# Kernel optimization log

Hardware: AMD Instinct MI355X
Metric: run time of the kernel (lower is better)

Reference implementation:

```python
import jax, jax.numpy as jnp
import numpy as np

B, IN_CH, OUT_CH, H, W = 2, 256, 128, 96, 96
KS = 3  # deformable kernel size


def _conv2d(x, w, b=None, stride=1, padding=0):
    out = jax.lax.conv_general_dilated(
        x, w, (stride, stride), [(padding, padding), (padding, padding)],
        dimension_numbers=('NCHW', 'OIHW', 'NCHW'))
    if b is not None:
        out = out + b[None, :, None, None]
    return out


def _up2_bilinear_ac(x):
    b, c, h, w = x.shape
    H2, W2 = 2 * h, 2 * w
    ys = jnp.arange(H2, dtype=x.dtype) * ((h - 1) / (H2 - 1))
    xs = jnp.arange(W2, dtype=x.dtype) * ((w - 1) / (W2 - 1))
    y0 = jnp.floor(ys).astype(jnp.int32); y1 = jnp.minimum(y0 + 1, h - 1)
    x0 = jnp.floor(xs).astype(jnp.int32); x1 = jnp.minimum(x0 + 1, w - 1)
    wy = (ys - y0.astype(x.dtype))[None, None, :, None]
    wx = (xs - x0.astype(x.dtype))[None, None, None, :]
    rows = x[:, :, y0, :] * (1 - wy) + x[:, :, y1, :] * wy
    return rows[:, :, :, x0] * (1 - wx) + rows[:, :, :, x1] * wx


def _deform_conv(x, pw, pb, cw, ks=3):
    # DeformConv2d with padding=0, stride=1, modulation=False
    b, c, Hx, Wx = x.shape
    N = ks * ks
    off = jnp.transpose(_conv2d(x, pw, pb, stride=1, padding=1), (0, 2, 3, 1))  # [b,h,w,2N]
    h, w = off.shape[1], off.shape[2]
    r = (ks - 1) // 2
    pn_x, pn_y = jnp.meshgrid(jnp.arange(-r, r + 1), jnp.arange(-r, r + 1), indexing='ij')
    # p = p_0 (starts at 1, per torch code) + p_n + offset; x-coord first half, y-coord second half
    px = off[..., :N] + pn_x.ravel().astype(x.dtype) + jnp.arange(1, h + 1, dtype=x.dtype)[None, :, None, None]
    py = off[..., N:] + pn_y.ravel().astype(x.dtype) + jnp.arange(1, w + 1, dtype=x.dtype)[None, None, :, None]
    fx, fy = jnp.floor(px), jnp.floor(py)  # detached in torch; floor grad is 0 anyway
    x_lt = jnp.clip(fx, 0, Hx - 1); y_lt = jnp.clip(fy, 0, Wx - 1)
    x_rb = jnp.clip(fx + 1, 0, Hx - 1); y_rb = jnp.clip(fy + 1, 0, Wx - 1)
    pxc = jnp.clip(px, 0, Hx - 1); pyc = jnp.clip(py, 0, Wx - 1)
    g_lt = (1 + (x_lt - pxc)) * (1 + (y_lt - pyc))
    g_rb = (1 - (x_rb - pxc)) * (1 - (y_rb - pyc))
    g_lb = (1 + (x_lt - pxc)) * (1 - (y_rb - pyc))
    g_rt = (1 - (x_rb - pxc)) * (1 + (y_lt - pyc))
    x_flat = x.reshape(b, c, Hx * Wx)
    gather = jax.vmap(lambda xf, ix: xf[:, ix])  # [c,HW],[M] -> [c,M], vmapped over batch

    def take(qx, qy):
        idx = (qx.astype(jnp.int32) * Wx + qy.astype(jnp.int32)).reshape(b, -1)
        return gather(x_flat, idx).reshape(b, c, h, w, N)

    x_off = (g_lt[:, None] * take(x_lt, y_lt) + g_rb[:, None] * take(x_rb, y_rb)
             + g_lb[:, None] * take(x_lt, y_rb) + g_rt[:, None] * take(x_rb, y_lt))
    # _reshape_x_offset: [b,c,h,w,kx,ky] -> [b,c,h*ks,w*ks]
    x_off = x_off.reshape(b, c, h, w, ks, ks).transpose(0, 1, 2, 4, 3, 5).reshape(b, c, h * ks, w * ks)
    return _conv2d(x_off, cw, stride=ks)  # kernel=ks, stride=ks, no bias


def _bn_relu(x, g, be, eps=1e-5):
    # training-mode BatchNorm2d (biased batch variance) + ReLU
    m = x.mean(axis=(0, 2, 3), keepdims=True)
    v = x.var(axis=(0, 2, 3), keepdims=True)
    return jax.nn.relu((x - m) / jnp.sqrt(v + eps) * g[None, :, None, None] + be[None, :, None, None])


def setup_inputs() -> dict:
    key = jax.random.key(0)
    ks = jax.random.split(key, 16)
    f = jnp.float32
    return {
        'x1': jax.random.normal(ks[0], (B, OUT_CH, H, W), f),
        'x2': jax.random.normal(ks[1], (B, IN_CH, H // 2, W // 2), f),
        'chW': jax.random.normal(ks[2], (OUT_CH, IN_CH, 3, 3), f) * 0.02,
        'chB': jnp.zeros((OUT_CH,), f),
        'p1W': jax.random.normal(ks[3], (2 * KS * KS, IN_CH, 3, 3), f) * 0.01,
        'p1B': jax.random.normal(ks[4], (2 * KS * KS,), f) * 0.01,
        'c1W': jax.random.normal(ks[5], (OUT_CH, IN_CH, KS, KS), f) * 0.02,
        'bn1g': jnp.ones((OUT_CH,), f),
        'bn1b': jnp.zeros((OUT_CH,), f),
        'p2W': jax.random.normal(ks[6], (2 * KS * KS, OUT_CH, 3, 3), f) * 0.01,
        'p2B': jax.random.normal(ks[7], (2 * KS * KS,), f) * 0.01,
        'c2W': jax.random.normal(ks[8], (OUT_CH, OUT_CH, KS, KS), f) * 0.02,
        'bn2g': jnp.ones((OUT_CH,), f),
        'bn2b': jnp.zeros((OUT_CH,), f),
    }


def reference(x1, x2, chW, chB, p1W, p1B, c1W, bn1g, bn1b, p2W, p2B, c2W, bn2g, bn2b):
    x2u = _up2_bilinear_ac(x2)                                    # [B,IN_CH,H,W]
    x2c = jax.nn.relu(_conv2d(x2u, chW, chB, stride=1, padding=1))  # halve_channel -> [B,OUT_CH,H,W]
    # F.pad of x1 is a no-op here (shapes already match)
    x = jnp.concatenate([x2c, x1], axis=1)                        # [B,IN_CH,H,W]
    y = _bn_relu(_deform_conv(x, p1W, p1B, c1W, KS), bn1g, bn1b)  # [B,OUT_CH,H,W]
    y = _bn_relu(_deform_conv(y, p2W, p2B, c2W, KS), bn2g, bn2b)  # [B,OUT_CH,H,W]
    return y
```

## Files before the change

### kernel.cpp

```cpp
#include <hip/hip_runtime.h>
#include <hip/hip_bf16.h>

#define Bn 2
#define INCH 256
#define OUTCH 128
#define Hs 96
#define Ws 96
#define HW (Hs*Ws)
#define N9 9

typedef __attribute__((ext_vector_type(8))) short bf16x8;
typedef __attribute__((ext_vector_type(4))) float f32x4;

static __device__ inline ushort bfbits(float v) {
    __hip_bfloat16 h = __float2bfloat16(v);
    return *reinterpret_cast<ushort*>(&h);
}
static __device__ inline float bf2f(ushort u) {
    __hip_bfloat16 h = *reinterpret_cast<__hip_bfloat16*>(&u);
    return __bfloat162float(h);
}
static __device__ inline uint packu(ushort lo, ushort hi) {
    return (uint)lo | ((uint)hi << 16);
}
static __device__ inline float rchi(uint u) { return __uint_as_float(u << 16); }
static __device__ inline float rclo(uint u) { return __uint_as_float(u & 0xffff0000u); }

template<int C>
__global__ void up2_nhwc_kernel(const float* __restrict__ in, uint* __restrict__ out) {
    __shared__ float t[32][33];
    constexpr int PB = HW / 32;
    int blk = blockIdx.x;
    int p0 = (blk % PB) * 32;
    int c0 = ((blk / PB) % (C / 32)) * 32;
    int b = blk / (PB * (C / 32));
    int tp = threadIdx.x & 31, tg = threadIdx.x >> 5;
    int p = p0 + tp;
    int xo = p % Ws, yo = p / Ws;
    const float s = 47.0f / 95.0f;
    float yf = yo * s, xf = xo * s;
    int y0 = (int)floorf(yf); int y1 = min(y0 + 1, 47);
    int x0 = (int)floorf(xf); int x1 = min(x0 + 1, 47);
    float wy = yf - (float)y0, wx = xf - (float)x0;
    #pragma unroll
    for (int r = 0; r < 4; r++) {
        int c = c0 + tg + r * 8;
        const float* pp = in + ((size_t)b * C + c) * 2304;
        float r0 = pp[y0*48 + x0] * (1.f - wy) + pp[y1*48 + x0] * wy;
        float r1 = pp[y0*48 + x1] * (1.f - wy) + pp[y1*48 + x1] * wy;
        t[tg + r * 8][tp] = r0 * (1.f - wx) + r1 * wx;
    }
    __syncthreads();
    #pragma unroll
    for (int r = 0; r < 4; r++) {
        int po = p0 + tg + r * 8;
        float v = t[tp][tg + r * 8];
        ushort h = bfbits(v);
        ushort l = bfbits(v - bf2f(h));
        out[((size_t)b * HW + po) * C + c0 + tp] = packu(h, l);
    }
}

__global__ void combine_t_kernel(const float* __restrict__ ph0, const float* __restrict__ ph1,
                                 const float* __restrict__ x1, const float* __restrict__ bias,
                                 float* __restrict__ xcat, uint* __restrict__ xcatT) {
    __shared__ float t[32][33];
    constexpr int PB = HW / 32;
    int blk = blockIdx.x;
    int p0 = (blk % PB) * 32;
    int c0 = ((blk / PB) % (INCH / 32)) * 32;
    int b = blk / (PB * (INCH / 32));
    int tp = threadIdx.x & 31, tg = threadIdx.x >> 5;
    #pragma unroll
    for (int r = 0; r < 4; r++) {
        int c = c0 + tg + r * 8;
        float v;
        if (c < OUTCH) {
            size_t i = ((size_t)b * OUTCH + c) * HW + p0 + tp;
            v = fmaxf(ph0[i] + ph1[i] + bias[c], 0.f);
        } else {
            v = x1[((size_t)b * OUTCH + (c - OUTCH)) * HW + p0 + tp];
        }
        t[tg + r * 8][tp] = v;
        xcat[((size_t)b * INCH + c) * HW + p0 + tp] = v;
    }
    __syncthreads();
    #pragma unroll
    for (int r = 0; r < 4; r++) {
        int po = p0 + tg + r * 8;
        float v = t[tp][tg + r * 8];
        ushort h = bfbits(v);
        ushort l = bfbits(v - bf2f(h));
        xcatT[((size_t)b * HW + po) * INCH + c0 + tp] = packu(h, l);
    }
}

__global__ void bnapply_t_kernel(const float* __restrict__ p0, const float* __restrict__ p1,
                                 const float* __restrict__ mv, const float* __restrict__ g,
                                 const float* __restrict__ be,
                                 float* __restrict__ y, uint* __restrict__ yT) {
    __shared__ float t[32][33];
    constexpr int PB = HW / 32;
    int blk = blockIdx.x;
    int p0x = (blk % PB) * 32;
    int c0 = ((blk / PB) % (OUTCH / 32)) * 32;
    int b = blk / (PB * (OUTCH / 32));
    int tp = threadIdx.x & 31, tg = threadIdx.x >> 5;
    #pragma unroll
    for (int r = 0; r < 4; r++) {
        int c = c0 + tg + r * 8;
        size_t i = ((size_t)b * OUTCH + c) * HW + p0x + tp;
        float m = mv[c], vv = mv[OUTCH + c];
        float x = p0[i] + p1[i];
        float rr = fmaxf((x - m) / sqrtf(vv + 1e-5f) * g[c] + be[c], 0.f);
        t[tg + r * 8][tp] = rr;
        y[i] = rr;
    }
    __syncthreads();
    #pragma unroll
    for (int r = 0; r < 4; r++) {
        int po = p0x + tg + r * 8;
        float v = t[tp][tg + r * 8];
        ushort h = bfbits(v);
        ushort l = bfbits(v - bf2f(h));
        yT[((size_t)b * HW + po) * OUTCH + c0 + tp] = packu(h, l);
    }
}

template<int CIN, int SPLIT>
__global__ void offconv_kernel(const float* __restrict__ in, const float* __restrict__ w,
                               float* __restrict__ part) {
    constexpr int CS = CIN / SPLIT;
    constexpr int BPS = Bn * HW / 256;
    int s = blockIdx.x / BPS;
    int p = (blockIdx.x % BPS) * 256 + threadIdx.x;
    int b = p / HW; int pin = p % HW;
    int i = pin / Ws, j = pin % Ws;
    const float* ib = in + ((size_t)b * CIN + s * CS) * HW;
    const float* wb = w + (size_t)s * CS * N9;
    float acc[18];
    #pragma unroll
    for (int o = 0; o < 18; o++) acc[o] = 0.f;
    for (int c = 0; c < CS; c++) {
        float v[9];
        #pragma unroll
        for (int n = 0; n < 9; n++) {
            int rr = i + n / 3 - 1, cc = j + n % 3 - 1;
            v[n] = (rr >= 0 && rr < Hs && cc >= 0 && cc < Ws) ? ib[(size_t)c * HW + rr * Ws + cc] : 0.f;
        }
        const float* wc = wb + (size_t)c * N9;
        #pragma unroll
        for (int o = 0; o < 18; o++) {
            #pragma unroll
            for (int n = 0; n < 9; n++) acc[o] += wc[(size_t)o * CIN * N9 + n] * v[n];
        }
    }
    #pragma unroll
    for (int o = 0; o < 18; o++)
        part[(((size_t)s * Bn + b) * 18 + o) * HW + pin] = acc[o];
}

template<int SPLIT>
__global__ void offreduce_kernel(const float* __restrict__ part, const float* __restrict__ bias,
                                 float* __restrict__ off) {
    int idx = blockIdx.x * blockDim.x + threadIdx.x;
    const int total = Bn * 18 * HW;
    if (idx >= total) return;
    int pin = idx % HW;
    int o = (idx / HW) % 18;
    int b = idx / (18 * HW);
    float a = bias[o];
    #pragma unroll
    for (int s = 0; s < SPLIT; s++) a += part[(((size_t)s * Bn + b) * 18 + o) * HW + pin];
    off[((size_t)b * 18 + o) * HW + pin] = a;
}

template<int CIN>
__global__ void wprep_big_kernel(const float* __restrict__ cw, ushort* __restrict__ wp) {
    int e = blockIdx.x * 256 + threadIdx.x;
    if (e >= CIN * 9 * 128) return;
    int kl = e & 31, oc = (e >> 5) & 127, k32 = e >> 12;
    int k = k32 * 32 + kl;
    int n = k / CIN, c = k & (CIN - 1);
    float v = cw[((size_t)oc * CIN + c) * 9 + n];
    ushort h = bfbits(v);
    wp[e] = h;
    wp[e + CIN * 9 * 128] = bfbits(v - bf2f(h));
}

__global__ void mkparams_kernel(const float* __restrict__ off, int4* __restrict__ pidx,
                                float4* __restrict__ pw) {
    int e = blockIdx.x * blockDim.x + threadIdx.x;
    const int total = Bn * HW * N9;
    if (e >= total) return;
    int n = e % N9;
    int p = e / N9;
    int j = p % Ws;
    int i = (p / Ws) % Hs;
    int b = p / HW;
    float ox = off[((size_t)b * 18 + n) * HW + i * Ws + j];
    float oy = off[((size_t)b * 18 + 9 + n) * HW + i * Ws + j];
    float px = ox + (float)(n / 3 - 1) + (float)(i + 1);
    float py = oy + (float)(n % 3 - 1) + (float)(j + 1);
    float fx = floorf(px), fy = floorf(py);
    float x_lt = fminf(fmaxf(fx,       0.f), 95.f);
    float x_rb = fminf(fmaxf(fx + 1.f, 0.f), 95.f);
    float y_lt = fminf(fmaxf(fy,       0.f), 95.f);
    float y_rb = fminf(fmaxf(fy + 1.f, 0.f), 95.f);
    float pxc  = fminf(fmaxf(px, 0.f), 95.f);
    float pyc  = fminf(fmaxf(py, 0.f), 95.f);
    float g_lt = (1.f + (x_lt - pxc)) * (1.f + (y_lt - pyc));
    float g_rb = (1.f - (x_rb - pxc)) * (1.f - (y_rb - pyc));
    float g_lb = (1.f + (x_lt - pxc)) * (1.f - (y_rb - pyc));
    float g_rt = (1.f - (x_rb - pxc)) * (1.f + (y_lt - pyc));
    int ilt = (int)x_lt * Ws + (int)y_lt;
    int irb = (int)x_rb * Ws + (int)y_rb;
    int ilb = (int)x_lt * Ws + (int)y_rb;
    int irt = (int)x_rb * Ws + (int)y_lt;
    pidx[e] = make_int4(ilt, irb, ilb, irt);
    pw[e]   = make_float4(g_lt, g_rb, g_lb, g_rt);
}

template<int CIN, bool DEFORM, bool SPLIT3>
__global__ void mgemm_big_kernel(const uint* __restrict__ xT, const ushort* __restrict__ wp,
                                 const int4* __restrict__ pidx, const float4* __restrict__ pw,
                                 float* __restrict__ p0, float* __restrict__ p1) {
    constexpr int KS = CIN * 9 / 2;
    constexpr int NSTEP = KS / 64;
    constexpr int PX = 32;
    constexpr int TILES = Bn * HW / PX;
    constexpr int CPX = 2 * TILES / 8;
    __shared__ ushort Ah[2][PX][80];
    __shared__ ushort Al[2][PX][80];
    __shared__ int4  sidx[PX * N9];
    __shared__ float4 ssw[PX * N9];

    int tid = threadIdx.x;
    int bid = blockIdx.x;
    int swz = (bid & 7) * CPX + (bid >> 3);
    int s = swz / TILES;
    int t = swz % TILES;
    int p0x = t * PX;
    int b = p0x / HW;
    int pin = p0x % HW;
    int irow = pin / Ws, j0 = pin % Ws;

    if constexpr (DEFORM) {
        for (int e = tid; e < PX * N9; e += 256) {
            sidx[e] = pidx[(size_t)p0x * N9 + e];
            ssw[e]  = pw[(size_t)p0x * N9 + e];
        }
        __syncthreads();
    }
    const uint* xbT = xT + (size_t)b * HW * CIN;
    const ushort* wlo = wp + (size_t)CIN * 9 * 128;
    int w = tid >> 6, lane = tid & 63;
    int lg = lane >> 4, l15 = lane & 15;
    int fpx = tid >> 4, fc4 = tid & 15;

    f32x4 acc[2][2];
    #pragma unroll
    for (int mf = 0; mf < 2; mf++)
        #pragma unroll
        for (int nf = 0; nf < 2; nf++) acc[mf][nf] = (f32x4){0.f, 0.f, 0.f, 0.f};
    int bswz0 = (l15 >> 2) << 3;
    int col0 = (fc4 * 4) ^ ((fpx >> 2) << 3);
    int col1 = (fc4 * 4) ^ (((fpx + 16) >> 2) << 3);

    uint4 qa0, qb0, qc0, qd0, qa1, qb1, qc1, qd1;
    auto gload = [&](int ks) {
        int k0 = s * KS + ks * 64;
        int n = k0 / CIN;
        int cc = (k0 & (CIN - 1)) + fc4 * 4;
        if constexpr (DEFORM) {
            int4 i4 = sidx[fpx * 9 + n];
            qa0 = *(const uint4*)&xbT[(size_t)i4.x * CIN + cc];
            qb0 = *(const uint4*)&xbT[(size_t)i4.y * CIN + cc];
            qc0 = *(const uint4*)&xbT[(size_t)i4.z * CIN + cc];
            qd0 = *(const uint4*)&xbT[(size_t)i4.w * CIN + cc];
            int4 j4 = sidx[(fpx + 16) * 9 + n];
            qa1 = *(const uint4*)&xbT[(size_t)j4.x * CIN + cc];
            qb1 = *(const uint4*)&xbT[(size_t)j4.y * CIN + cc];
            qc1 = *(const uint4*)&xbT[(size_t)j4.z * CIN + cc];
            qd1 = *(const uint4*)&xbT[(size_t)j4.w * CIN + cc];
        } else {
            int n3 = n / 3;
            int rr = irow + n3 - 1;
            int cl0 = j0 + fpx + (n - 3 * n3) - 1;
            qa0 = make_uint4(0u, 0u, 0u, 0u);
            qa1 = make_uint4(0u, 0u, 0u, 0u);
            if (rr >= 0 && rr < Hs) {
                if (cl0 >= 0 && cl0 < Ws)
                    qa0 = *(const uint4*)&xbT[(size_t)(rr * Ws + cl0) * CIN + cc];
                if (cl0 + 16 >= 0 && cl0 + 16 < Ws)
                    qa1 = *(const uint4*)&xbT[(size_t)(rr * Ws + cl0 + 16) * CIN + cc];
            }
        }
    };
    auto bil4 = [&](const uint4& A, const uint4& B, const uint4& C, const uint4& D,
                    const float4& w4, ushort* hh, ushort* ll) {
        const uint ua[4] = {A.x, A.y, A.z, A.w}, ub[4] = {B.x, B.y, B.z, B.w},
                   uc[4] = {C.x, C.y, C.z, C.w}, ud[4] = {D.x, D.y, D.z, D.w};
        #pragma unroll
        for (int j = 0; j < 4; j++) {
            float v = w4.x * (rchi(ua[j]) + rclo(ua[j])) + w4.y * (rchi(ub[j]) + rclo(ub[j]))
                    + w4.z * (rchi(uc[j]) + rclo(uc[j])) + w4.w * (rchi(ud[j]) + rclo(ud[j]));
            hh[j] = bfbits(v);
            if constexpr (SPLIT3) ll[j] = bfbits(v - bf2f(hh[j]));
        }
    };
    gload(0);

    for (int ks = 0; ks < NSTEP; ks++) {
        int k0 = s * KS + ks * 64;
        int cur = ks & 1;
        ushort h0[4], l0[4], h1[4], l1[4];
        if constexpr (DEFORM) {
            int n = k0 / CIN;
            float4 wA = ssw[fpx * 9 + n];
            float4 wB = ssw[(fpx + 16) * 9 + n];
            bil4(qa0, qb0, qc0, qd0, wA, h0, l0);
            bil4(qa1, qb1, qc1, qd1, wB, h1, l1);
        } else {
            const uint u0[4] = {qa0.x, qa0.y, qa0.z, qa0.w};
            const uint u1[4] = {qa1.x, qa1.y, qa1.z, qa1.w};
            #pragma unroll
            for (int j = 0; j < 4; j++) {
                h0[j] = (ushort)(u0[j] & 0xffffu);
                h1[j] = (ushort)(u1[j] & 0xffffu);
                if constexpr (SPLIT3) {
                    l0[j] = (ushort)(u0[j] >> 16);
                    l1[j] = (ushort)(u1[j] >> 16);
                }
            }
        }
        if (ks + 1 < NSTEP) gload(ks + 1);
        {
            uint2 v0; v0.x = packu(h0[0], h0[1]); v0.y = packu(h0[2], h0[3]);
            uint2 v1; v1.x = packu(h1[0], h1[1]); v1.y = packu(h1[2], h1[3]);
            *(uint2*)&Ah[cur][fpx][col0] = v0;
            *(uint2*)&Ah[cur][fpx + 16][col1] = v1;
            if constexpr (SPLIT3) {
                uint2 w0; w0.x = packu(l0[0], l0[1]); w0.y = packu(l0[2], l0[3]);
                uint2 w1; w1.x = packu(l1[0], l1[1]); w1.y = packu(l1[2], l1[3]);
                *(uint2*)&Al[cur][fpx][col0] = w0;
                *(uint2*)&Al[cur][fpx + 16][col1] = w1;
            }
        }
        __syncthreads();
        #pragma unroll
        for (int kk = 0; kk < 2; kk++) {
            const ushort* wpk = wp + ((size_t)(k0 / 32 + kk) * 128) * 32;
            int bc0 = (kk * 32 + lg * 8) ^ bswz0;
            int bc1 = bc0 ^ 32;
            bf16x8 a0h = *(const bf16x8*)&wpk[(32 * w + l15) * 32 + lg * 8];
            bf16x8 a1h = *(const bf16x8*)&wpk[(32 * w + 16 + l15) * 32 + lg * 8];
            bf16x8 b0h = *(const bf16x8*)&Ah[cur][l15][bc0];
            bf16x8 b1h = *(const bf16x8*)&Ah[cur][16 + l15][bc1];
            acc[0][0] = __builtin_amdgcn_mfma_f32_16x16x32_bf16(a0h, b0h, acc[0][0], 0, 0, 0);
            acc[0][1] = __builtin_amdgcn_mfma_f32_16x16x32_bf16(a0h, b1h, acc[0][1], 0, 0, 0);
            acc[1][0] = __builtin_amdgcn_mfma_f32_16x16x32_bf16(a1h, b0h, acc[1][0], 0, 0, 0);
            acc[1][1] = __builtin_amdgcn_mfma_f32_16x16x32_bf16(a1h, b1h, acc[1][1], 0, 0, 0);
            if constexpr (SPLIT3) {
                const ushort* wpl = wlo + ((size_t)(k0 / 32 + kk) * 128) * 32;
                bf16x8 a0l = *(const bf16x8*)&wpl[(32 * w + l15) * 32 + lg * 8];
                bf16x8 a1l = *(const bf16x8*)&wpl[(32 * w + 16 + l15) * 32 + lg * 8];
                bf16x8 b0l = *(const bf16x8*)&Al[cur][l15][bc0];
                bf16x8 b1l = *(const bf16x8*)&Al[cur][16 + l15][bc1];
                acc[0][0] = __builtin_amdgcn_mfma_f32_16x16x32_bf16(a0h, b0l, acc[0][0], 0, 0, 0);
                acc[0][0] = __builtin_amdgcn_mfma_f32_16x16x32_bf16(a0l, b0h, acc[0][0], 0, 0, 0);
                acc[0][1] = __builtin_amdgcn_mfma_f32_16x16x32_bf16(a0h, b1l, acc[0][1], 0, 0, 0);
                acc[0][1] = __builtin_amdgcn_mfma_f32_16x16x32_bf16(a0l, b1h, acc[0][1], 0, 0, 0);
                acc[1][0] = __builtin_amdgcn_mfma_f32_16x16x32_bf16(a1h, b0l, acc[1][0], 0, 0, 0);
                acc[1][0] = __builtin_amdgcn_mfma_f32_16x16x32_bf16(a1l, b0h, acc[1][0], 0, 0, 0);
                acc[1][1] = __builtin_amdgcn_mfma_f32_16x16x32_bf16(a1h, b1l, acc[1][1], 0, 0, 0);
                acc[1][1] = __builtin_amdgcn_mfma_f32_16x16x32_bf16(a1l, b1h, acc[1][1], 0, 0, 0);
            }
        }
    }
    float* pout = s ? p1 : p0;
    #pragma unroll
    for (int mf = 0; mf < 2; mf++) {
        int oc = 32 * w + 16 * mf + lg * 4;
        #pragma unroll
        for (int nf = 0; nf < 2; nf++) {
            #pragma unroll
            for (int r = 0; r < 4; r++)
                pout[((size_t)b * OUTCH + oc + r) * HW + pin + nf * 16 + l15] = acc[mf][nf][r];
        }
    }
}

__global__ void bnstats_kernel(const float* __restrict__ p0, const float* __restrict__ p1,
                               float* __restrict__ mv) {
    int o = blockIdx.x;
    int tid = threadIdx.x;
    float s = 0.f, sq = 0.f;
    for (int k = tid; k < Bn * HW; k += 256) {
        int b = k / HW, p = k % HW;
        size_t idx = ((size_t)b * OUTCH + o) * HW + p;
        float v = p0[idx] + p1[idx];
        s += v; sq += v * v;
    }
    __shared__ float rs[256], rq[256];
    rs[tid] = s; rq[tid] = sq;
    __syncthreads();
    for (int st = 128; st > 0; st >>= 1) {
        if (tid < st) { rs[tid] += rs[tid + st]; rq[tid] += rq[tid + st]; }
        __syncthreads();
    }
    if (tid == 0) {
        float m = rs[0] / (float)(Bn * HW);
        mv[o] = m;
        mv[OUTCH + o] = rq[0] / (float)(Bn * HW) - m * m;
    }
}

__global__ void bnapply_kernel(const float* __restrict__ p0, const float* __restrict__ p1,
                               const float* __restrict__ mv,
                               const float* __restrict__ g, const float* __restrict__ be,
                               float* __restrict__ y) {
    int idx = blockIdx.x * blockDim.x + threadIdx.x;
    const int total = Bn * OUTCH * HW;
    if (idx >= total) return;
    int o = (idx / HW) % OUTCH;
    float m = mv[o], v = mv[OUTCH + o];
    float x = p0[idx] + p1[idx];
    float r = (x - m) / sqrtf(v + 1e-5f) * g[o] + be[o];
    y[idx] = fmaxf(r, 0.f);
}

extern "C" void kernel_launch(void* const* d_in, const int* in_sizes, int n_in,
                              void* d_out, int out_size, void* d_ws, size_t ws_size,
                              hipStream_t stream) {
    const float* x1   = (const float*)d_in[0];
    const float* x2   = (const float*)d_in[1];
    const float* chW  = (const float*)d_in[2];
    const float* chB  = (const float*)d_in[3];
    const float* p1W  = (const float*)d_in[4];
    const float* p1B  = (const float*)d_in[5];
    const float* c1W  = (const float*)d_in[6];
    const float* bn1g = (const float*)d_in[7];
    const float* bn1b = (const float*)d_in[8];
    const float* p2W  = (const float*)d_in[9];
    const float* p2B  = (const float*)d_in[10];
    const float* c2W  = (const float*)d_in[11];
    const float* bn2g = (const float*)d_in[12];
    const float* bn2b = (const float*)d_in[13];
    float* out = (float*)d_out;

    float* ws = (float*)d_ws;
    uint*  x2uT  = (uint*)(ws + 9437184);
    ushort* cwThb = (ushort*)(ws + 4718592);
    float* p0h   = ws;
    float* p1h   = ws + 2359296;
    float* xcat  = ws + 4718592;
    uint*  xcatT = (uint*)(ws + 9437184);

    float* part1 = ws;
    float* offb1 = ws + 2654208;
    int4*  pidx1 = (int4*)(ws + 2985984);
    float4* pw41 = (float4*)(ws + 3649536);
    ushort* cwTb1 = (ushort*)(ws + 4313088);
    float* p0d1  = ws + 4718592;
    float* p1d1  = ws + 4718592 + 2359296;
    float* y1    = ws;
    uint*  y1T   = (uint*)(ws + 9437184);

    float* part2 = ws + 4718592;
    float* offb2 = ws + 4718592 + 2654208;
    int4*  pidx2 = (int4*)(ws + 4718592 + 2985984);
    float4* pw42 = (float4*)(ws + 4718592 + 3649536);
    ushort* cwTb2 = (ushort*)(ws + 4718592 + 4313088);
    float* p0d2  = ws;
    float* p1d2  = ws + 2359296;
    float* mv    = ws + 14155776;

    constexpr int BIG_GRID = 2 * Bn * HW / 32;
    constexpr int UP_GRID  = (HW/32) * (INCH/32) * Bn;
    constexpr int CT_GRID  = (HW/32) * (INCH/32) * Bn;
    constexpr int BT_GRID  = (HW/32) * (OUTCH/32) * Bn;

    up2_nhwc_kernel<INCH><<<UP_GRID, 256, 0, stream>>>(x2, x2uT);
    wprep_big_kernel<INCH><<<(INCH*9*128 + 255) / 256, 256, 0, stream>>>(chW, cwThb);
    mgemm_big_kernel<INCH, false, true><<<BIG_GRID, 256, 0, stream>>>(x2uT, cwThb, nullptr, nullptr, p0h, p1h);
    combine_t_kernel<<<CT_GRID, 256, 0, stream>>>(p0h, p1h, x1, chB, xcat, xcatT);

    offconv_kernel<INCH, 8><<<8 * (Bn*HW/256), 256, 0, stream>>>(xcat, p1W, part1);
    offreduce_kernel<8><<<(Bn*18*HW + 255) / 256, 256, 0, stream>>>(part1, p1B, offb1);
    mkparams_kernel<<<(Bn*HW*N9 + 255) / 256, 256, 0, stream>>>(offb1, pidx1, pw41);
    wprep_big_kernel<INCH><<<(INCH*9*128 + 255) / 256, 256, 0, stream>>>(c1W, cwTb1);
    mgemm_big_kernel<INCH, true, true><<<BIG_GRID, 256, 0, stream>>>(xcatT, cwTb1, pidx1, pw41, p0d1, p1d1);
    bnstats_kernel<<<OUTCH, 256, 0, stream>>>(p0d1, p1d1, mv);
    bnapply_t_kernel<<<BT_GRID, 256, 0, stream>>>(p0d1, p1d1, mv, bn1g, bn1b, y1, y1T);

    offconv_kernel<OUTCH, 8><<<8 * (Bn*HW/256), 256, 0, stream>>>(y1, p2W, part2);
    offreduce_kernel<8><<<(Bn*18*HW + 255) / 256, 256, 0, stream>>>(part2, p2B, offb2);
    mkparams_kernel<<<(Bn*HW*N9 + 255) / 256, 256, 0, stream>>>(offb2, pidx2, pw42);
    wprep_big_kernel<OUTCH><<<(OUTCH*9*128 + 255) / 256, 256, 0, stream>>>(c2W, cwTb2);
    mgemm_big_kernel<OUTCH, true, false><<<BIG_GRID, 256, 0, stream>>>(y1T, cwTb2, pidx2, pw42, p0d2, p1d2);
    bnstats_kernel<<<OUTCH, 256, 0, stream>>>(p0d2, p1d2, mv);
    bnapply_kernel<<<(Bn*OUTCH*HW + 255) / 256, 256, 0, stream>>>(p0d2, p1d2, mv, bn2g, bn2b, out);
}
```

Measured before the change: 358.5 us.

## Fuse sampling params into second deform GEMM with three-way K split

The second deformable conv now computes its bilinear indices and weights inline from the offset buffer, which removes the mkparams kernel and its pidx/pw4 round trip through memory. The K dimension is split three ways instead of two, giving more blocks, and the BN stats and apply kernels now sum three partial buffers. The cost is recomputing the parameters in each block, a third partial buffer to write and read, and a simpler single-precision bf16 MFMA path without the hi/lo split.

```diff
diff --git a/kernel.cpp b/kernel.cpp
--- a/kernel.cpp
+++ b/kernel.cpp
@@ -25,6 +25,30 @@
 }
 static __device__ inline float rchi(uint u) { return __uint_as_float(u << 16); }
 static __device__ inline float rclo(uint u) { return __uint_as_float(u & 0xffff0000u); }
+
+static __device__ inline void mkpar(const float* __restrict__ off, int b, int n, int pp,
+                                    int4& i4, float4& w4) {
+    int i = pp / Ws, j = pp % Ws;
+    float ox = off[((size_t)(b * 18 + n)) * HW + pp];
+    float oy = off[((size_t)(b * 18 + 9 + n)) * HW + pp];
+    float px = ox + (float)(n / 3 - 1) + (float)(i + 1);
+    float py = oy + (float)(n % 3 - 1) + (float)(j + 1);
+    float fx = floorf(px), fy = floorf(py);
+    float x_lt = fminf(fmaxf(fx,       0.f), 95.f);
+    float x_rb = fminf(fmaxf(fx + 1.f, 0.f), 95.f);
+    float y_lt = fminf(fmaxf(fy,       0.f), 95.f);
+    float y_rb = fminf(fmaxf(fy + 1.f, 0.f), 95.f);
+    float pxc  = fminf(fmaxf(px, 0.f), 95.f);
+    float pyc  = fminf(fmaxf(py, 0.f), 95.f);
+    w4.x = (1.f + (x_lt - pxc)) * (1.f + (y_lt - pyc));
+    w4.y = (1.f - (x_rb - pxc)) * (1.f - (y_rb - pyc));
+    w4.z = (1.f + (x_lt - pxc)) * (1.f - (y_rb - pyc));
+    w4.w = (1.f - (x_rb - pxc)) * (1.f + (y_lt - pyc));
+    i4.x = (int)x_lt * Ws + (int)y_lt;
+    i4.y = (int)x_rb * Ws + (int)y_rb;
+    i4.z = (int)x_lt * Ws + (int)y_rb;
+    i4.w = (int)x_rb * Ws + (int)y_lt;
+}
 
 template<int C>
 __global__ void up2_nhwc_kernel(const float* __restrict__ in, uint* __restrict__ out) {
@@ -391,6 +415,123 @@
     }
 }
 
+template<int CIN>
+__global__ void mgemm_d3_kernel(const uint* __restrict__ xT, const ushort* __restrict__ wp,
+                                const float* __restrict__ offb,
+                                float* __restrict__ q0, float* __restrict__ q1,
+                                float* __restrict__ q2) {
+    constexpr int KS = CIN * 3;
+    constexpr int NSTEP = KS / 64;
+    constexpr int PX = 32;
+    constexpr int TILES = Bn * HW / PX;
+    constexpr int CPX = 3 * TILES / 8;
+    __shared__ ushort Ah[2][PX][80];
+
+    int tid = threadIdx.x;
+    int bid = blockIdx.x;
+    int swz = (bid & 7) * CPX + (bid >> 3);
+    int s = swz / TILES;
+    int t = swz % TILES;
+    int p0x = t * PX;
+    int b = p0x / HW;
+    int pin = p0x % HW;
+
+    const uint* xbT = xT + (size_t)b * HW * CIN;
+    int w = tid >> 6, lane = tid & 63;
+    int lg = lane >> 4, l15 = lane & 15;
+    int fpx = tid >> 4, fc4 = tid & 15;
+    int pp0 = pin + fpx, pp1 = pin + fpx + 16;
+
+    f32x4 acc[2][2];
+    #pragma unroll
+    for (int mf = 0; mf < 2; mf++)
+        #pragma unroll
+        for (int nf = 0; nf < 2; nf++) acc[mf][nf] = (f32x4){0.f, 0.f, 0.f, 0.f};
+    int bswz0 = (l15 >> 2) << 3;
+    int col0 = (fc4 * 4) ^ ((fpx >> 2) << 3);
+    int col1 = (fc4 * 4) ^ (((fpx + 16) >> 2) << 3);
+
+    int4 ia0, ia1; float4 wa0, wa1;
+    int ncur = (s * KS) / CIN;
+    mkpar(offb, b, ncur, pp0, ia0, wa0);
+    mkpar(offb, b, ncur, pp1, ia1, wa1);
+
+    uint4 qa0, qb0, qc0, qd0, qa1, qb1, qc1, qd1;
+    auto gload = [&](int ks) {
+        int k0 = s * KS + ks * 64;
+        int cc = (k0 & (CIN - 1)) + fc4 * 4;
+        qa0 = *(const uint4*)&xbT[(size_t)ia0.x * CIN + cc];
+        qb0 = *(const uint4*)&xbT[(size_t)ia0.y * CIN + cc];
+        qc0 = *(const uint4*)&xbT[(size_t)ia0.z * CIN + cc];
+        qd0 = *(const uint4*)&xbT[(size_t)ia0.w * CIN + cc];
+        qa1 = *(const uint4*)&xbT[(size_t)ia1.x * CIN + cc];
+        qb1 = *(const uint4*)&xbT[(size_t)ia1.y * CIN + cc];
+        qc1 = *(const uint4*)&xbT[(size_t)ia1.z * CIN + cc];
+        qd1 = *(const uint4*)&xbT[(size_t)ia1.w * CIN + cc];
+    };
+    auto bil4h = [&](const uint4& A, const uint4& B, const uint4& C, const uint4& D,
+                     const float4& w4, ushort* hh) {
+        const uint ua[4] = {A.x, A.y, A.z, A.w}, ub[4] = {B.x, B.y, B.z, B.w},
+                   uc[4] = {C.x, C.y, C.z, C.w}, ud[4] = {D.x, D.y, D.z, D.w};
+        #pragma unroll
+        for (int j = 0; j < 4; j++) {
+            float v = w4.x * (rchi(ua[j]) + rclo(ua[j])) + w4.y * (rchi(ub[j]) + rclo(ub[j]))
+                    + w4.z * (rchi(uc[j]) + rclo(uc[j])) + w4.w * (rchi(ud[j]) + rclo(ud[j]));
+            hh[j] = bfbits(v);
+        }
+    };
+    gload(0);
+
+    for (int ks = 0; ks < NSTEP; ks++) {
+        int k0 = s * KS + ks * 64;
+        int cur = ks & 1;
+        ushort h0[4], h1[4];
+        bil4h(qa0, qb0, qc0, qd0, wa0, h0);
+        bil4h(qa1, qb1, qc1, qd1, wa1, h1);
+        if (ks + 1 < NSTEP) {
+            int nn = (k0 + 64) / CIN;
+            if (nn != ncur) {
+                ncur = nn;
+                mkpar(offb, b, ncur, pp0, ia0, wa0);
+                mkpar(offb, b, ncur, pp1, ia1, wa1);
+            }
+            gload(ks + 1);
+        }
+        {
+            uint2 v0; v0.x = packu(h0[0], h0[1]); v0.y = packu(h0[2], h0[3]);
+            uint2 v1; v1.x = packu(h1[0], h1[1]); v1.y = packu(h1[2], h1[3]);
+            *(uint2*)&Ah[cur][fpx][col0] = v0;
+            *(uint2*)&Ah[cur][fpx + 16][col1] = v1;
+        }
+        __syncthreads();
+        #pragma unroll
+        for (int kk = 0; kk < 2; kk++) {
+            const ushort* wpk = wp + ((size_t)(k0 / 32 + kk) * 128) * 32;
+            int bc0 = (kk * 32 + lg * 8) ^ bswz0;
+            int bc1 = bc0 ^ 32;
+            bf16x8 a0h = *(const bf16x8*)&wpk[(32 * w + l15) * 32 + lg * 8];
+            bf16x8 a1h = *(const bf16x8*)&wpk[(32 * w + 16 + l15) * 32 + lg * 8];
+            bf16x8 b0h = *(const bf16x8*)&Ah[cur][l15][bc0];
+            bf16x8 b1h = *(const bf16x8*)&Ah[cur][16 + l15][bc1];
+            acc[0][0] = __builtin_amdgcn_mfma_f32_16x16x32_bf16(a0h, b0h, acc[0][0], 0, 0, 0);
+            acc[0][1] = __builtin_amdgcn_mfma_f32_16x16x32_bf16(a0h, b1h, acc[0][1], 0, 0, 0);
+            acc[1][0] = __builtin_amdgcn_mfma_f32_16x16x32_bf16(a1h, b0h, acc[1][0], 0, 0, 0);
+            acc[1][1] = __builtin_amdgcn_mfma_f32_16x16x32_bf16(a1h, b1h, acc[1][1], 0, 0, 0);
+        }
+    }
+    float* pout = (s == 0) ? q0 : (s == 1) ? q1 : q2;
+    #pragma unroll
+    for (int mf = 0; mf < 2; mf++) {
+        int oc = 32 * w + 16 * mf + lg * 4;
+        #pragma unroll
+        for (int nf = 0; nf < 2; nf++) {
+            #pragma unroll
+            for (int r = 0; r < 4; r++)
+                pout[((size_t)b * OUTCH + oc + r) * HW + pin + nf * 16 + l15] = acc[mf][nf][r];
+        }
+    }
+}
+
 __global__ void bnstats_kernel(const float* __restrict__ p0, const float* __restrict__ p1,
                                float* __restrict__ mv) {
     int o = blockIdx.x;
@@ -416,16 +557,41 @@
     }
 }
 
-__global__ void bnapply_kernel(const float* __restrict__ p0, const float* __restrict__ p1,
-                               const float* __restrict__ mv,
-                               const float* __restrict__ g, const float* __restrict__ be,
-                               float* __restrict__ y) {
+__global__ void bnstats3_kernel(const float* __restrict__ q0, const float* __restrict__ q1,
+                                const float* __restrict__ q2, float* __restrict__ mv) {
+    int o = blockIdx.x;
+    int tid = threadIdx.x;
+    float s = 0.f, sq = 0.f;
+    for (int k = tid; k < Bn * HW; k += 256) {
+        int b = k / HW, p = k % HW;
+        size_t idx = ((size_t)b * OUTCH + o) * HW + p;
+        float v = q0[idx] + q1[idx] + q2[idx];
+        s += v; sq += v * v;
+    }
+    __shared__ float rs[256], rq[256];
+    rs[tid] = s; rq[tid] = sq;
+    __syncthreads();
+    for (int st = 128; st > 0; st >>= 1) {
+        if (tid < st) { rs[tid] += rs[tid + st]; rq[tid] += rq[tid + st]; }
+        __syncthreads();
+    }
+    if (tid == 0) {
+        float m = rs[0] / (float)(Bn * HW);
+        mv[o] = m;
+        mv[OUTCH + o] = rq[0] / (float)(Bn * HW) - m * m;
+    }
+}
+
+__global__ void bnapply3_kernel(const float* __restrict__ q0, const float* __restrict__ q1,
+                                const float* __restrict__ q2, const float* __restrict__ mv,
+                                const float* __restrict__ g, const float* __restrict__ be,
+                                float* __restrict__ y) {
     int idx = blockIdx.x * blockDim.x + threadIdx.x;
     const int total = Bn * OUTCH * HW;
     if (idx >= total) return;
     int o = (idx / HW) % OUTCH;
     float m = mv[o], v = mv[OUTCH + o];
-    float x = p0[idx] + p1[idx];
+    float x = q0[idx] + q1[idx] + q2[idx];
     float r = (x - m) / sqrtf(v + 1e-5f) * g[o] + be[o];
     y[idx] = fmaxf(r, 0.f);
 }
@@ -450,41 +616,43 @@
     float* out = (float*)d_out;
 
     float* ws = (float*)d_ws;
-    uint*  x2uT  = (uint*)(ws + 9437184);
-    ushort* cwThb = (ushort*)(ws + 4718592);
-    float* p0h   = ws;
-    float* p1h   = ws + 2359296;
-    float* xcat  = ws + 4718592;
-    uint*  xcatT = (uint*)(ws + 9437184);
+    constexpr size_t P = 2359296;
+    uint*  x2uT  = (uint*)(ws + 4 * P);
+    ushort* cwThb = (ushort*)(ws + 2 * P);
+    float* qh0   = ws;
+    float* qh1   = ws + P;
+    float* xcat  = ws + 2 * P;
+    uint*  xcatT = (uint*)(ws + 4 * P);
 
     float* part1 = ws;
     float* offb1 = ws + 2654208;
     int4*  pidx1 = (int4*)(ws + 2985984);
     float4* pw41 = (float4*)(ws + 3649536);
     ushort* cwTb1 = (ushort*)(ws + 4313088);
-    float* p0d1  = ws + 4718592;
-    float* p1d1  = ws + 4718592 + 2359296;
+    float* p0d1  = ws + 2 * P;
+    float* p1d1  = ws + 3 * P;
     float* y1    = ws;
-    uint*  y1T   = (uint*)(ws + 9437184);
-
-    float* part2 = ws + 4718592;
-    float* offb2 = ws + 4718592 + 2654208;
-    int4*  pidx2 = (int4*)(ws + 4718592 + 2985984);
-    float4* pw42 = (float4*)(ws + 4718592 + 3649536);
-    ushort* cwTb2 = (ushort*)(ws + 4718592 + 4313088);
-    float* p0d2  = ws;
-    float* p1d2  = ws + 2359296;
-    float* mv    = ws + 14155776;
-
-    constexpr int BIG_GRID = 2 * Bn * HW / 32;
+    uint*  y1T   = (uint*)(ws + 4 * P);
+
+    float* part2 = ws + 2 * P;
+    float* offb2 = ws + 2 * P + 2654208;
+    ushort* cwTb2 = (ushort*)(ws + 2 * P + 4313088);
+    float* q0d2  = ws;
+    float* q1d2  = ws + P;
+    float* q2d2  = ws + 5 * P;
+    float* mv    = ws + 6 * P;
+
+    constexpr int TILES = Bn * HW / 32;
+    constexpr int BIG_GRID = 2 * TILES;
+    constexpr int D3_GRID  = 3 * TILES;
     constexpr int UP_GRID  = (HW/32) * (INCH/32) * Bn;
     constexpr int CT_GRID  = (HW/32) * (INCH/32) * Bn;
     constexpr int BT_GRID  = (HW/32) * (OUTCH/32) * Bn;
 
     up2_nhwc_kernel<INCH><<<UP_GRID, 256, 0, stream>>>(x2, x2uT);
     wprep_big_kernel<INCH><<<(INCH*9*128 + 255) / 256, 256, 0, stream>>>(chW, cwThb);
-    mgemm_big_kernel<INCH, false, true><<<BIG_GRID, 256, 0, stream>>>(x2uT, cwThb, nullptr, nullptr, p0h, p1h);
-    combine_t_kernel<<<CT_GRID, 256, 0, stream>>>(p0h, p1h, x1, chB, xcat, xcatT);
+    mgemm_big_kernel<INCH, false, true><<<BIG_GRID, 256, 0, stream>>>(x2uT, cwThb, nullptr, nullptr, qh0, qh1);
+    combine_t_kernel<<<CT_GRID, 256, 0, stream>>>(qh0, qh1, x1, chB, xcat, xcatT);
 
     offconv_kernel<INCH, 8><<<8 * (Bn*HW/256), 256, 0, stream>>>(xcat, p1W, part1);
     offreduce_kernel<8><<<(Bn*18*HW + 255) / 256, 256, 0, stream>>>(part1, p1B, offb1);
@@ -496,9 +664,8 @@
 
     offconv_kernel<OUTCH, 8><<<8 * (Bn*HW/256), 256, 0, stream>>>(y1, p2W, part2);
     offreduce_kernel<8><<<(Bn*18*HW + 255) / 256, 256, 0, stream>>>(part2, p2B, offb2);
-    mkparams_kernel<<<(Bn*HW*N9 + 255) / 256, 256, 0, stream>>>(offb2, pidx2, pw42);
     wprep_big_kernel<OUTCH><<<(OUTCH*9*128 + 255) / 256, 256, 0, stream>>>(c2W, cwTb2);
-    mgemm_big_kernel<OUTCH, true, false><<<BIG_GRID, 256, 0, stream>>>(y1T, cwTb2, pidx2, pw42, p0d2, p1d2);
-    bnstats_kernel<<<OUTCH, 256, 0, stream>>>(p0d2, p1d2, mv);
-    bnapply_kernel<<<(Bn*OUTCH*HW + 255) / 256, 256, 0, stream>>>(p0d2, p1d2, mv, bn2g, bn2b, out);
-}
+    mgemm_d3_kernel<OUTCH><<<D3_GRID, 256, 0, stream>>>(y1T, cwTb2, offb2, q0d2, q1d2, q2d2);
+    bnstats3_kernel<<<OUTCH, 256, 0, stream>>>(q0d2, q1d2, q2d2, mv);
+    bnapply3_kernel<<<(Bn*OUTCH*HW + 255) / 256, 256, 0, stream>>>(q0d2, q1d2, q2d2, mv, bn2g, bn2b, out);
+}
```

New measurement: 355.2 us. Within noise of the previous version (-0.9%).
